# Kernel optimization log

Hardware: AMD Instinct MI355X
Metric: run time of the kernel (lower is better)

## Reference

```python
import jax, jax.numpy as jnp
import numpy as np

B, T, IN_DIM, OUT_DIM, H = 4096, 256, 64, 32, 128

def _linear_params(key, out_f, in_f):
    k1, k2 = jax.random.split(key)
    bound = 1.0 / np.sqrt(in_f)
    W = jax.random.uniform(k1, (out_f, in_f), jnp.float32, -bound, bound)
    b = jax.random.uniform(k2, (out_f,), jnp.float32, -bound, bound)
    return W, b

def _lstm_params(key, input_sz, hidden_sz):
    ks = jax.random.split(key, 4)
    bound = 1.0 / np.sqrt(hidden_sz)
    Wih = jax.random.uniform(ks[0], (4 * hidden_sz, input_sz), jnp.float32, -bound, bound)
    Whh = jax.random.uniform(ks[1], (4 * hidden_sz, hidden_sz), jnp.float32, -bound, bound)
    bih = jax.random.uniform(ks[2], (4 * hidden_sz,), jnp.float32, -bound, bound)
    bhh = jax.random.uniform(ks[3], (4 * hidden_sz,), jnp.float32, -bound, bound)
    return Wih, Whh, bih, bhh

def setup_inputs() -> dict:
    key = jax.random.key(0)
    ks = jax.random.split(key, 9)
    seq = jax.random.normal(ks[0], (B, T, IN_DIM), jnp.float32)
    h1 = jnp.zeros((B, H), jnp.float32); c1 = jnp.zeros((B, H), jnp.float32)
    h2 = jnp.zeros((B, H), jnp.float32); c2 = jnp.zeros((B, H), jnp.float32)
    W_in1, b_in1 = _linear_params(ks[1], 256, IN_DIM)
    W_in2, b_in2 = _linear_params(ks[2], 128, 256)
    W_in3, b_in3 = _linear_params(ks[3], 128, 128)
    Wih1, Whh1, bih1, bhh1 = _lstm_params(ks[4], 128, H)
    Wih2, Whh2, bih2, bhh2 = _lstm_params(ks[5], 128, H)
    W_out1, b_out1 = _linear_params(ks[6], 128, 128)
    W_out2, b_out2 = _linear_params(ks[7], 256, 128)
    W_out3, b_out3 = _linear_params(ks[8], OUT_DIM, 256)
    return dict(seq=seq, h1=h1, c1=c1, h2=h2, c2=c2,
                W_in1=W_in1, b_in1=b_in1, W_in2=W_in2, b_in2=b_in2, W_in3=W_in3, b_in3=b_in3,
                Wih1=Wih1, Whh1=Whh1, bih1=bih1, bhh1=bhh1,
                Wih2=Wih2, Whh2=Whh2, bih2=bih2, bhh2=bhh2,
                W_out1=W_out1, b_out1=b_out1, W_out2=W_out2, b_out2=b_out2, W_out3=W_out3, b_out3=b_out3)

def _lstm_cell(x, h, c, Wih, Whh, bih, bhh):
    # PyTorch LSTMCell: gates ordered i, f, g, o
    g = x @ Wih.T + bih + h @ Whh.T + bhh
    i, f, gg, o = jnp.split(g, 4, axis=-1)
    c_new = jax.nn.sigmoid(f) * c + jax.nn.sigmoid(i) * jnp.tanh(gg)
    h_new = jax.nn.sigmoid(o) * jnp.tanh(c_new)
    return h_new, c_new

def reference(seq, h1, c1, h2, c2,
              W_in1, b_in1, W_in2, b_in2, W_in3, b_in3,
              Wih1, Whh1, bih1, bhh1, Wih2, Whh2, bih2, bhh2,
              W_out1, b_out1, W_out2, b_out2, W_out3, b_out3):
    # fc_in applied to all timesteps at once (same math as per-step)
    x = jax.nn.relu(seq @ W_in1.T + b_in1)
    x = jax.nn.relu(x @ W_in2.T + b_in2)
    x = jax.nn.relu(x @ W_in3.T + b_in3)  # [B, T, 128]

    def step(carry, xt):
        h1, c1, h2, c2 = carry
        h1, c1 = _lstm_cell(xt, h1, c1, Wih1, Whh1, bih1, bhh1)
        h2, c2 = _lstm_cell(h1, h2, c2, Wih2, Whh2, bih2, bhh2)
        return (h1, c1, h2, c2), None

    (h1, c1, h2, c2), _ = jax.lax.scan(step, (h1, c1, h2, c2), jnp.swapaxes(x, 0, 1))

    y = jax.nn.relu(h2 @ W_out1.T + b_out1)
    y = jax.nn.relu(y @ W_out2.T + b_out2)
    return y @ W_out3.T + b_out3  # [B, out_dim]
```

## Files before the change

### kernel.cpp

```cpp
#include <hip/hip_runtime.h>


typedef unsigned short u16;
typedef short bf16x8 __attribute__((ext_vector_type(8)));
typedef float f32x4 __attribute__((ext_vector_type(4)));
typedef unsigned short u16x4 __attribute__((ext_vector_type(4)));

#define MFMA16(a, b, c) __builtin_amdgcn_mfma_f32_16x16x32_bf16((a), (b), (c), 0, 0, 0)

#define GLOAD_LDS(gp, lp) __builtin_amdgcn_global_load_lds( \
    (const __attribute__((address_space(1))) unsigned int*)(const void*)(gp), \
    (__attribute__((address_space(3))) unsigned int*)(void*)(lp), 16, 0, 0)

#define LGKM_BAR do { \
  asm volatile("s_waitcnt lgkmcnt(0)" ::: "memory"); \
  __builtin_amdgcn_sched_barrier(0); \
  __builtin_amdgcn_s_barrier(); \
  __builtin_amdgcn_sched_barrier(0); \
} while (0)

__device__ __forceinline__ u16 f2bf(float f) {
  union { float f; unsigned u; } v; v.f = f;
  return (u16)((v.u + 0x7FFFu + ((v.u >> 16) & 1u)) >> 16);
}
__device__ __forceinline__ float fsig(float x) { return 1.0f / (1.0f + __expf(-x)); }
__device__ __forceinline__ float ftanh(float x) { return 2.0f / (1.0f + __expf(-2.0f * x)) - 1.0f; }

#define WC1_U   0
#define WC2V_U  131072
#define WC2L_U  196608
#define W1_U    262144
#define W2_U    278528
#define W3_U    311296
#define WO1_U   327680
#define WO2_U   344064
#define WO3_U   376832
#define BS1_F   192512
#define BS2_F   193024
#define STH1_U  393216
#define STH2_U  917504
#define C1_F    720896
#define C2_F    1245184
#define XB_U    4194304
#define TC      32
#define NCH     8

__global__ void prep_kernel(const float* __restrict__ Wih1, const float* __restrict__ Whh1,
                            const float* __restrict__ bih1, const float* __restrict__ bhh1,
                            const float* __restrict__ Wih2, const float* __restrict__ Whh2,
                            const float* __restrict__ bih2, const float* __restrict__ bhh2,
                            const float* __restrict__ W_in1, const float* __restrict__ W_in2,
                            const float* __restrict__ W_in3,
                            const float* __restrict__ W_out1, const float* __restrict__ W_out2,
                            const float* __restrict__ W_out3,
                            const float* __restrict__ h1_in, const float* __restrict__ h2_in,
                            const float* __restrict__ c1_in, const float* __restrict__ c2_in,
                            u16* __restrict__ wsu) {
  float* wsf = (float*)wsu;
  const int N_total = 2490368;
  int stride = gridDim.x * blockDim.x;
  for (int idx = blockIdx.x * blockDim.x + threadIdx.x; idx < N_total; idx += stride) {
    if (idx < 385024) {
      int within = idx & 511;
      int frag = (idx >> 9);
      int lane = within >> 3, e = within & 7;
      int lr = lane & 15, lg = lane >> 4;
      int k8 = lg * 8 + e;
      float v;
      if (idx < 131072) {
        int kf = frag & 7, g = (frag >> 3) & 3, w = frag >> 5;
        int row = g * 128 + w * 16 + lr;
        int k = kf * 32 + k8;
        v = (k < 128) ? Wih1[row * 128 + k] : Whh1[row * 128 + (k - 128)];
      } else if (idx < 196608) {
        int f = frag - 256;
        int kf = f & 3, g = (f >> 2) & 3, w = f >> 4;
        v = Wih2[(g * 128 + w * 16 + lr) * 128 + kf * 32 + k8];
      } else if (idx < 262144) {
        int f = frag - 384;
        int kf = f & 3, g = (f >> 2) & 3, w = f >> 4;
        v = Whh2[(g * 128 + w * 16 + lr) * 128 + kf * 32 + k8];
      } else if (idx < 278528) {
        int f = frag - 512; int kf = f & 1, n = f >> 1;
        v = W_in1[(n * 16 + lr) * 64 + kf * 32 + k8];
      } else if (idx < 311296) {
        int f = frag - 544; int kf = f & 7, n = f >> 3;
        v = W_in2[(n * 16 + lr) * 256 + kf * 32 + k8];
      } else if (idx < 327680) {
        int f = frag - 608; int kf = f & 3, n = f >> 2;
        v = W_in3[(n * 16 + lr) * 128 + kf * 32 + k8];
      } else if (idx < 344064) {
        int f = frag - 640; int kf = f & 3, n = f >> 2;
        v = W_out1[(n * 16 + lr) * 128 + kf * 32 + k8];
      } else if (idx < 376832) {
        int f = frag - 672; int kf = f & 3, n = f >> 2;
        v = W_out2[(n * 16 + lr) * 128 + kf * 32 + k8];
      } else {
        int f = frag - 736; int kf = f & 7, n = f >> 3;
        v = W_out3[(n * 16 + lr) * 256 + kf * 32 + k8];
      }
      wsu[idx] = f2bf(v);
    } else if (idx < 385536) {
      int i = idx - 385024; wsf[BS1_F + i] = bih1[i] + bhh1[i];
    } else if (idx < 386048) {
      int i = idx - 385536; wsf[BS2_F + i] = bih2[i] + bhh2[i];
    } else if (idx < 393216) {
    } else if (idx < 917504) {
      int i = idx - 393216; wsu[STH1_U + i] = f2bf(h1_in[i]);
    } else if (idx < 1441792) {
      int i = idx - 917504; wsu[STH2_U + i] = f2bf(h2_in[i]);
    } else if (idx < 1966080) {
      int i = idx - 1441792; wsf[C1_F + i] = c1_in[i];
    } else {
      int i = idx - 1966080; wsf[C2_F + i] = c2_in[i];
    }
  }
}

__global__ __launch_bounds__(256, 2)
void fc_chunk(const float* __restrict__ seq,
              const float* __restrict__ b_in1, const float* __restrict__ b_in2,
              const float* __restrict__ b_in3,
              u16* __restrict__ wsu, int t0) {
  __shared__ u16 SEQs[4096];
  __shared__ u16 F1s[16384];
  __shared__ u16 F2s[8192];
  const int tid = threadIdx.x;
  const int wid = tid >> 6, lane = tid & 63;
  const int lr = lane & 15, lg = lane >> 4;
  const int bid = blockIdx.x;

#pragma unroll
  for (int i = 0; i < 4; ++i) {
    int f = i * 1024 + tid * 4;
    int rho = f >> 6, k = f & 63;
    int b = bid * 2 + (rho >> 5), tl = rho & 31;
    float4 v = *(const float4*)(seq + ((size_t)b * 256 + t0 + tl) * 64 + k);
    u16x4 o = { f2bf(v.x), f2bf(v.y), f2bf(v.z), f2bf(v.w) };
    *(u16x4*)&SEQs[(rho * 64 + k) ^ ((rho & 7) << 3)] = o;
  }
  __syncthreads();

  {
    f32x4 a1[4][4] = {};
#pragma unroll
    for (int kf = 0; kf < 2; ++kf) {
      bf16x8 A[4];
#pragma unroll
      for (int rt = 0; rt < 4; ++rt) {
        int r = 16 * rt + lr;
        A[rt] = *(const bf16x8*)&SEQs[(r * 64 + (kf * 4 + lg) * 8) ^ ((r & 7) << 3)];
      }
#pragma unroll
      for (int n = 0; n < 4; ++n) {
        bf16x8 B = *(const bf16x8*)(wsu + W1_U + (size_t)(((4 * wid + n) * 2 + kf) * 512) + lane * 8);
#pragma unroll
        for (int rt = 0; rt < 4; ++rt) a1[rt][n] = MFMA16(A[rt], B, a1[rt][n]);
      }
    }
#pragma unroll
    for (int n = 0; n < 4; ++n) {
      float bb = b_in1[(4 * wid + n) * 16 + lr];
#pragma unroll
      for (int rt = 0; rt < 4; ++rt)
#pragma unroll
        for (int j = 0; j < 4; ++j) {
          int r = 16 * rt + lg * 4 + j, c = (4 * wid + n) * 16 + lr;
          F1s[(r * 256 + c) ^ ((r & 7) << 3)] = f2bf(fmaxf(a1[rt][n][j] + bb, 0.f));
        }
    }
  }
  __syncthreads();

  {
    f32x4 a2[4][2] = {};
#pragma unroll
    for (int kf = 0; kf < 8; ++kf) {
      bf16x8 A[4];
#pragma unroll
      for (int rt = 0; rt < 4; ++rt) {
        int r = 16 * rt + lr;
        A[rt] = *(const bf16x8*)&F1s[(r * 256 + (kf * 4 + lg) * 8) ^ ((r & 7) << 3)];
      }
#pragma unroll
      for (int n = 0; n < 2; ++n) {
        bf16x8 B = *(const bf16x8*)(wsu + W2_U + (size_t)(((2 * wid + n) * 8 + kf) * 512) + lane * 8);
#pragma unroll
        for (int rt = 0; rt < 4; ++rt) a2[rt][n] = MFMA16(A[rt], B, a2[rt][n]);
      }
    }
#pragma unroll
    for (int n = 0; n < 2; ++n) {
      float bb = b_in2[(2 * wid + n) * 16 + lr];
#pragma unroll
      for (int rt = 0; rt < 4; ++rt)
#pragma unroll
        for (int j = 0; j < 4; ++j) {
          int r = 16 * rt + lg * 4 + j, c = (2 * wid + n) * 16 + lr;
          F2s[(r * 128 + c) ^ ((r & 7) << 3)] = f2bf(fmaxf(a2[rt][n][j] + bb, 0.f));
        }
    }
  }
  __syncthreads();

  {
    f32x4 a3[4][2] = {};
#pragma unroll
    for (int kf = 0; kf < 4; ++kf) {
      bf16x8 A[4];
#pragma unroll
      for (int rt = 0; rt < 4; ++rt) {
        int r = 16 * rt + lr;
        A[rt] = *(const bf16x8*)&F2s[(r * 128 + (kf * 4 + lg) * 8) ^ ((r & 7) << 3)];
      }
#pragma unroll
      for (int n = 0; n < 2; ++n) {
        bf16x8 B = *(const bf16x8*)(wsu + W3_U + (size_t)(((2 * wid + n) * 4 + kf) * 512) + lane * 8);
#pragma unroll
        for (int rt = 0; rt < 4; ++rt) a3[rt][n] = MFMA16(A[rt], B, a3[rt][n]);
      }
    }
#pragma unroll
    for (int n = 0; n < 2; ++n) {
      float bb = b_in3[(2 * wid + n) * 16 + lr];
#pragma unroll
      for (int rt = 0; rt < 4; ++rt)
#pragma unroll
        for (int j = 0; j < 4; ++j) {
          int rho = 16 * rt + lg * 4 + j;
          int b = bid * 2 + (rho >> 5), tl = rho & 31;
          int c = (2 * wid + n) * 16 + lr;
          wsu[XB_U + ((size_t)tl * 4096 + b) * 128 + c] = f2bf(fmaxf(a3[rt][n][j] + bb, 0.f));
        }
    }
  }
}

__global__ __launch_bounds__(512, 2)
void scan_chunk(u16* __restrict__ wsu, float* __restrict__ out,
                const float* __restrict__ b_out1, const float* __restrict__ b_out2,
                const float* __restrict__ b_out3, int last) {
  __shared__ u16 Wl[65536];
  __shared__ u16 XBs[2048];
  __shared__ u16 H1d[2][2048], H2d[2][2048];

  float* wsf = (float*)wsu;
  const int tid = threadIdx.x;
  const int wid = tid >> 6, lane = tid & 63;
  const int lr = lane & 15, lg = lane >> 4;
  const int b0 = blockIdx.x * 16;
  const int r5 = tid >> 5, c5 = (tid & 31) * 4;

  bf16x8 wgt1[4][8], wgt2v[4][4];
#pragma unroll
  for (int g = 0; g < 4; ++g) {
#pragma unroll
    for (int kf = 0; kf < 8; ++kf)
      wgt1[g][kf] = *(const bf16x8*)(wsu + WC1_U + (size_t)(((wid * 4 + g) * 8 + kf) * 512) + lane * 8);
#pragma unroll
    for (int kf = 0; kf < 4; ++kf)
      wgt2v[g][kf] = *(const bf16x8*)(wsu + WC2V_U + (size_t)(((wid * 4 + g) * 4 + kf) * 512) + lane * 8);
  }
#pragma unroll
  for (int g = 0; g < 4; ++g) {
#pragma unroll
    for (int kf = 0; kf < 8; ++kf) asm volatile("" : "+v"(wgt1[g][kf]));
#pragma unroll
    for (int kf = 0; kf < 4; ++kf) asm volatile("" : "+v"(wgt2v[g][kf]));
  }

#pragma unroll
  for (int i = 0; i < 16; ++i)
    GLOAD_LDS(wsu + WC2L_U + wid * 8192 + i * 512 + lane * 8, &Wl[wid * 8192 + i * 512]);

  u16x4 hh1 = *(const u16x4*)(wsu + STH1_U + (size_t)(b0 + r5) * 128 + c5);
  u16x4 hh2 = *(const u16x4*)(wsu + STH2_U + (size_t)(b0 + r5) * 128 + c5);
  u16x4 xq  = *(const u16x4*)(wsu + XB_U + ((size_t)0 * 4096 + b0 + r5) * 128 + c5);
  float cs1[4], cs2[4], bc1[4], bc2[4];
#pragma unroll
  for (int j = 0; j < 4; ++j) {
    cs1[j] = wsf[C1_F + (size_t)(b0 + lg * 4 + j) * 128 + 16 * wid + lr];
    cs2[j] = wsf[C2_F + (size_t)(b0 + lg * 4 + j) * 128 + 16 * wid + lr];
  }
#pragma unroll
  for (int g = 0; g < 4; ++g) {
    bc1[g] = wsf[BS1_F + g * 128 + 16 * wid + lr];
    bc2[g] = wsf[BS2_F + g * 128 + 16 * wid + lr];
  }
  {
    int sw = (r5 * 128 + c5) ^ ((r5 & 7) << 3);
    *(u16x4*)&H1d[0][sw] = hh1;
    *(u16x4*)&H2d[0][sw] = hh2;
    *(u16x4*)&XBs[sw] = xq;
  }
  __syncthreads();

#pragma unroll 2
  for (int tl = 0; tl < TC; ++tl) {
    const int p = tl & 1, q = p ^ 1;
    const bool ld = (tl < TC - 1);
    u16x4 xn;
    if (ld) xn = *(const u16x4*)(wsu + XB_U + ((size_t)(tl + 1) * 4096 + b0 + r5) * 128 + c5);

    f32x4 acc[4] = {};
#pragma unroll
    for (int kf = 0; kf < 8; ++kf) {
      const u16* ab = (kf < 4) ? XBs : H1d[p];
      int kg = (kf & 3) * 4 + lg;
      bf16x8 A = *(const bf16x8*)&ab[(lr * 128 + kg * 8) ^ ((lr & 7) << 3)];
#pragma unroll
      for (int g = 0; g < 4; ++g) acc[g] = MFMA16(A, wgt1[g][kf], acc[g]);
    }
    u16 hv[4];
#pragma unroll
    for (int j = 0; j < 4; ++j) {
      float gi = acc[0][j] + bc1[0];
      float gf = acc[1][j] + bc1[1];
      float gg = acc[2][j] + bc1[2];
      float go = acc[3][j] + bc1[3];
      float cn = fsig(gf) * cs1[j] + fsig(gi) * ftanh(gg);
      cs1[j] = cn;
      hv[j] = f2bf(fsig(go) * ftanh(cn));
    }
#pragma unroll
    for (int j = 0; j < 4; ++j) {
      int r = lg * 4 + j;
      H1d[q][(r * 128 + 16 * wid + lr) ^ ((r & 7) << 3)] = hv[j];
    }
    LGKM_BAR;

    f32x4 acd[4] = {};
#pragma unroll
    for (int kf = 0; kf < 4; ++kf) {
      int kg = kf * 4 + lg;
      bf16x8 A = *(const bf16x8*)&H1d[q][(lr * 128 + kg * 8) ^ ((lr & 7) << 3)];
#pragma unroll
      for (int g = 0; g < 4; ++g) acd[g] = MFMA16(A, wgt2v[g][kf], acd[g]);
    }
#pragma unroll
    for (int kf = 0; kf < 4; ++kf) {
      int kg = kf * 4 + lg;
      bf16x8 A = *(const bf16x8*)&H2d[p][(lr * 128 + kg * 8) ^ ((lr & 7) << 3)];
#pragma unroll
      for (int g = 0; g < 4; ++g) {
        bf16x8 B = *(const bf16x8*)&Wl[(size_t)(((wid * 4 + g) * 4 + kf) * 512) + lane * 8];
        acd[g] = MFMA16(A, B, acd[g]);
      }
    }
#pragma unroll
    for (int j = 0; j < 4; ++j) {
      float gi = acd[0][j] + bc2[0];
      float gf = acd[1][j] + bc2[1];
      float gg = acd[2][j] + bc2[2];
      float go = acd[3][j] + bc2[3];
      float cn = fsig(gf) * cs2[j] + fsig(gi) * ftanh(gg);
      cs2[j] = cn;
      hv[j] = f2bf(fsig(go) * ftanh(cn));
    }
#pragma unroll
    for (int j = 0; j < 4; ++j) {
      int r = lg * 4 + j;
      H2d[q][(r * 128 + 16 * wid + lr) ^ ((r & 7) << 3)] = hv[j];
    }
    if (ld) *(u16x4*)&XBs[(r5 * 128 + c5) ^ ((r5 & 7) << 3)] = xn;
    LGKM_BAR;
  }

  if (!last) {
    int sw = (r5 * 128 + c5) ^ ((r5 & 7) << 3);
    *(u16x4*)(wsu + STH1_U + (size_t)(b0 + r5) * 128 + c5) = *(const u16x4*)&H1d[0][sw];
    *(u16x4*)(wsu + STH2_U + (size_t)(b0 + r5) * 128 + c5) = *(const u16x4*)&H2d[0][sw];
#pragma unroll
    for (int j = 0; j < 4; ++j) {
      wsf[C1_F + (size_t)(b0 + lg * 4 + j) * 128 + 16 * wid + lr] = cs1[j];
      wsf[C2_F + (size_t)(b0 + lg * 4 + j) * 128 + 16 * wid + lr] = cs2[j];
    }
  } else {
    {
      f32x4 y1 = {};
#pragma unroll
      for (int kf = 0; kf < 4; ++kf) {
        int kg = kf * 4 + lg;
        bf16x8 A = *(const bf16x8*)&H2d[0][(lr * 128 + kg * 8) ^ ((lr & 7) << 3)];
        bf16x8 B = *(const bf16x8*)(wsu + WO1_U + (size_t)((wid * 4 + kf) * 512) + lane * 8);
        y1 = MFMA16(A, B, y1);
      }
      float bo1 = b_out1[wid * 16 + lr];
      LGKM_BAR;
#pragma unroll
      for (int j = 0; j < 4; ++j) {
        int r = lg * 4 + j;
        XBs[(r * 128 + 16 * wid + lr) ^ ((r & 7) << 3)] = f2bf(fmaxf(y1[j] + bo1, 0.f));
      }
      LGKM_BAR;
    }
    {
      f32x4 y2[2] = {};
#pragma unroll
      for (int kf = 0; kf < 4; ++kf) {
        int kg = kf * 4 + lg;
        bf16x8 A = *(const bf16x8*)&XBs[(lr * 128 + kg * 8) ^ ((lr & 7) << 3)];
#pragma unroll
        for (int n = 0; n < 2; ++n) {
          bf16x8 B = *(const bf16x8*)(wsu + WO2_U + (size_t)(((2 * wid + n) * 4 + kf) * 512) + lane * 8);
          y2[n] = MFMA16(A, B, y2[n]);
        }
      }
      LGKM_BAR;
#pragma unroll
      for (int n = 0; n < 2; ++n)
#pragma unroll
        for (int j = 0; j < 4; ++j) {
          int c = (2 * wid + n) * 16 + lr;
          float v = fmaxf(y2[n][j] + b_out2[c], 0.f);
          u16* buf = (c < 128) ? XBs : &H1d[0][0];
          int cc = c & 127, r = lg * 4 + j;
          buf[(r * 128 + cc) ^ ((r & 7) << 3)] = f2bf(v);
        }
      LGKM_BAR;
    }
    if (wid < 2) {
      f32x4 y3 = {};
#pragma unroll
      for (int kf = 0; kf < 8; ++kf) {
        const u16* ab = (kf < 4) ? XBs : &H1d[0][0];
        int kg = (kf & 3) * 4 + lg;
        bf16x8 A = *(const bf16x8*)&ab[(lr * 128 + kg * 8) ^ ((lr & 7) << 3)];
        bf16x8 B = *(const bf16x8*)(wsu + WO3_U + (size_t)((wid * 8 + kf) * 512) + lane * 8);
        y3 = MFMA16(A, B, y3);
      }
      float bo3 = b_out3[wid * 16 + lr];
#pragma unroll
      for (int j = 0; j < 4; ++j)
        out[(size_t)(b0 + lg * 4 + j) * 32 + wid * 16 + lr] = y3[j] + bo3;
    }
  }
}

extern "C" void kernel_launch(void* const* d_in, const int* in_sizes, int n_in,
                              void* d_out, int out_size, void* d_ws, size_t ws_size,
                              hipStream_t stream) {
  (void)in_sizes; (void)n_in; (void)out_size; (void)ws_size;
  const float* seq    = (const float*)d_in[0];
  const float* h1     = (const float*)d_in[1];
  const float* c1     = (const float*)d_in[2];
  const float* h2     = (const float*)d_in[3];
  const float* c2     = (const float*)d_in[4];
  const float* W_in1  = (const float*)d_in[5];
  const float* b_in1  = (const float*)d_in[6];
  const float* W_in2  = (const float*)d_in[7];
  const float* b_in2  = (const float*)d_in[8];
  const float* W_in3  = (const float*)d_in[9];
  const float* b_in3  = (const float*)d_in[10];
  const float* Wih1   = (const float*)d_in[11];
  const float* Whh1   = (const float*)d_in[12];
  const float* bih1   = (const float*)d_in[13];
  const float* bhh1   = (const float*)d_in[14];
  const float* Wih2   = (const float*)d_in[15];
  const float* Whh2   = (const float*)d_in[16];
  const float* bih2   = (const float*)d_in[17];
  const float* bhh2   = (const float*)d_in[18];
  const float* W_out1 = (const float*)d_in[19];
  const float* b_out1 = (const float*)d_in[20];
  const float* W_out2 = (const float*)d_in[21];
  const float* b_out2 = (const float*)d_in[22];
  const float* W_out3 = (const float*)d_in[23];
  const float* b_out3 = (const float*)d_in[24];
  u16* wsu = (u16*)d_ws;
  float* out = (float*)d_out;

  hipLaunchKernelGGL(prep_kernel, dim3(512), dim3(256), 0, stream,
                     Wih1, Whh1, bih1, bhh1, Wih2, Whh2, bih2, bhh2,
                     W_in1, W_in2, W_in3, W_out1, W_out2, W_out3,
                     h1, h2, c1, c2, wsu);
  for (int k = 0; k < NCH; ++k) {
    hipLaunchKernelGGL(fc_chunk, dim3(2048), dim3(256), 0, stream,
                       seq, b_in1, b_in2, b_in3, wsu, k * TC);
    hipLaunchKernelGGL(scan_chunk, dim3(256), dim3(512), 0, stream,
                       wsu, out, b_out1, b_out2, b_out3, (k == NCH - 1) ? 1 : 0);
  }
}
```

Before: 1.609 ms.

## Skew LSTM layers across timesteps to halve per-step barriers

Restructures the recurrent loop so layer 2 at step t and layer 1 at step t+1 run in the same iteration. Both read the same h1 fragments, so one barrier per timestep suffices instead of two, with a prologue and epilogue handling the first and last steps. X is double-buffered and prefetched two steps ahead, biases are folded into the accumulator initial values, and launch bounds drop to one block per CU, giving the compiler more registers. The risk is lower occupancy, added register pressure from holding h1 fragments across the skewed computation, and the complexity of the edge handling.

Result: slower. 2.096 ms (+30.3%).

```diff
diff --git a/kernel.cpp b/kernel.cpp
--- a/kernel.cpp
+++ b/kernel.cpp
@@ -236,13 +236,13 @@
   }
 }
 
-__global__ __launch_bounds__(512, 2)
+__global__ __launch_bounds__(512, 1)
 void scan_chunk(u16* __restrict__ wsu, float* __restrict__ out,
                 const float* __restrict__ b_out1, const float* __restrict__ b_out2,
                 const float* __restrict__ b_out3, int last) {
   __shared__ u16 Wl[65536];
-  __shared__ u16 XBs[2048];
-  __shared__ u16 H1d[2][2048], H2d[2][2048];
+  __shared__ u16 XB[2][2048];
+  __shared__ u16 H1b[2][2048], H2b[2][2048];
 
   float* wsf = (float*)wsu;
   const int tid = threadIdx.x;
@@ -250,6 +250,7 @@
   const int lr = lane & 15, lg = lane >> 4;
   const int b0 = blockIdx.x * 16;
   const int r5 = tid >> 5, c5 = (tid & 31) * 4;
+  const int swl = (r5 * 128 + c5) ^ ((r5 & 7) << 3);
 
   bf16x8 wgt1[4][8], wgt2v[4][4];
 #pragma unroll
@@ -273,9 +274,11 @@
   for (int i = 0; i < 16; ++i)
     GLOAD_LDS(wsu + WC2L_U + wid * 8192 + i * 512 + lane * 8, &Wl[wid * 8192 + i * 512]);
 
-  u16x4 hh1 = *(const u16x4*)(wsu + STH1_U + (size_t)(b0 + r5) * 128 + c5);
-  u16x4 hh2 = *(const u16x4*)(wsu + STH2_U + (size_t)(b0 + r5) * 128 + c5);
-  u16x4 xq  = *(const u16x4*)(wsu + XB_U + ((size_t)0 * 4096 + b0 + r5) * 128 + c5);
+  *(u16x4*)&H1b[0][swl] = *(const u16x4*)(wsu + STH1_U + (size_t)(b0 + r5) * 128 + c5);
+  *(u16x4*)&H2b[1][swl] = *(const u16x4*)(wsu + STH2_U + (size_t)(b0 + r5) * 128 + c5);
+  *(u16x4*)&XB[0][swl]  = *(const u16x4*)(wsu + XB_U + ((size_t)0 * 4096 + b0 + r5) * 128 + c5);
+  *(u16x4*)&XB[1][swl]  = *(const u16x4*)(wsu + XB_U + ((size_t)1 * 4096 + b0 + r5) * 128 + c5);
+
   float cs1[4], cs2[4], bc1[4], bc2[4];
 #pragma unroll
   for (int j = 0; j < 4; ++j) {
@@ -287,152 +290,191 @@
     bc1[g] = wsf[BS1_F + g * 128 + 16 * wid + lr];
     bc2[g] = wsf[BS2_F + g * 128 + 16 * wid + lr];
   }
-  {
-    int sw = (r5 * 128 + c5) ^ ((r5 & 7) << 3);
-    *(u16x4*)&H1d[0][sw] = hh1;
-    *(u16x4*)&H2d[0][sw] = hh2;
-    *(u16x4*)&XBs[sw] = xq;
-  }
   __syncthreads();
 
-#pragma unroll 2
-  for (int tl = 0; tl < TC; ++tl) {
-    const int p = tl & 1, q = p ^ 1;
-    const bool ld = (tl < TC - 1);
-    u16x4 xn;
-    if (ld) xn = *(const u16x4*)(wsu + XB_U + ((size_t)(tl + 1) * 4096 + b0 + r5) * 128 + c5);
-
-    f32x4 acc[4] = {};
-#pragma unroll
-    for (int kf = 0; kf < 8; ++kf) {
-      const u16* ab = (kf < 4) ? XBs : H1d[p];
-      int kg = (kf & 3) * 4 + lg;
-      bf16x8 A = *(const bf16x8*)&ab[(lr * 128 + kg * 8) ^ ((lr & 7) << 3)];
-#pragma unroll
-      for (int g = 0; g < 4; ++g) acc[g] = MFMA16(A, wgt1[g][kf], acc[g]);
-    }
-    u16 hv[4];
+  auto frag = [&](const u16* buf, int kg) -> bf16x8 {
+    return *(const bf16x8*)&buf[(lr * 128 + kg * 8) ^ ((lr & 7) << 3)];
+  };
+  auto ew = [&](f32x4 (&a)[4], float (&cs)[4], u16 (&hv)[4]) {
 #pragma unroll
     for (int j = 0; j < 4; ++j) {
-      float gi = acc[0][j] + bc1[0];
-      float gf = acc[1][j] + bc1[1];
-      float gg = acc[2][j] + bc1[2];
-      float go = acc[3][j] + bc1[3];
-      float cn = fsig(gf) * cs1[j] + fsig(gi) * ftanh(gg);
-      cs1[j] = cn;
-      hv[j] = f2bf(fsig(go) * ftanh(cn));
-    }
+      float cn = fsig(a[1][j]) * cs[j] + fsig(a[0][j]) * ftanh(a[2][j]);
+      cs[j] = cn;
+      hv[j] = f2bf(fsig(a[3][j]) * ftanh(cn));
+    }
+  };
+  auto hwrite = [&](u16* buf, const u16 (&hv)[4]) {
 #pragma unroll
     for (int j = 0; j < 4; ++j) {
       int r = lg * 4 + j;
-      H1d[q][(r * 128 + 16 * wid + lr) ^ ((r & 7) << 3)] = hv[j];
-    }
+      buf[(r * 128 + 16 * wid + lr) ^ ((r & 7) << 3)] = hv[j];
+    }
+  };
+
+  {
+    f32x4 a1[4];
+#pragma unroll
+    for (int g = 0; g < 4; ++g) a1[g] = (f32x4){bc1[g], bc1[g], bc1[g], bc1[g]};
+    bf16x8 h1f[4];
+#pragma unroll
+    for (int kf = 0; kf < 4; ++kf) h1f[kf] = frag(H1b[0], kf * 4 + lg);
+#pragma unroll
+    for (int kf = 0; kf < 4; ++kf) {
+      bf16x8 xf = frag(XB[0], kf * 4 + lg);
+#pragma unroll
+      for (int g = 0; g < 4; ++g) a1[g] = MFMA16(xf, wgt1[g][kf], a1[g]);
+    }
+#pragma unroll
+    for (int kf = 0; kf < 4; ++kf)
+#pragma unroll
+      for (int g = 0; g < 4; ++g) a1[g] = MFMA16(h1f[kf], wgt1[g][4 + kf], a1[g]);
+    u16 hv[4];
+    ew(a1, cs1, hv);
     LGKM_BAR;
-
-    f32x4 acd[4] = {};
+    hwrite(H1b[0], hv);
+    LGKM_BAR;
+  }
+
+#pragma unroll 2
+  for (int tl = 0; tl < TC - 1; ++tl) {
+    const int p = tl & 1, q = p ^ 1;
+    int tn = tl + 2; if (tn > TC - 1) tn = TC - 1;
+    u16x4 xn = *(const u16x4*)(wsu + XB_U + ((size_t)tn * 4096 + b0 + r5) * 128 + c5);
+
+    bf16x8 h1f[4];
+#pragma unroll
+    for (int kf = 0; kf < 4; ++kf) h1f[kf] = frag(H1b[p], kf * 4 + lg);
+
+    f32x4 a2[4];
+#pragma unroll
+    for (int g = 0; g < 4; ++g) a2[g] = (f32x4){bc2[g], bc2[g], bc2[g], bc2[g]};
+#pragma unroll
+    for (int kf = 0; kf < 4; ++kf)
+#pragma unroll
+      for (int g = 0; g < 4; ++g) a2[g] = MFMA16(h1f[kf], wgt2v[g][kf], a2[g]);
 #pragma unroll
     for (int kf = 0; kf < 4; ++kf) {
-      int kg = kf * 4 + lg;
-      bf16x8 A = *(const bf16x8*)&H1d[q][(lr * 128 + kg * 8) ^ ((lr & 7) << 3)];
-#pragma unroll
-      for (int g = 0; g < 4; ++g) acd[g] = MFMA16(A, wgt2v[g][kf], acd[g]);
-    }
+      bf16x8 h2f = frag(H2b[q], kf * 4 + lg);
+#pragma unroll
+      for (int g = 0; g < 4; ++g) {
+        bf16x8 B = *(const bf16x8*)&Wl[(((wid * 4 + g) * 4 + kf) * 512) + lane * 8];
+        a2[g] = MFMA16(h2f, B, a2[g]);
+      }
+    }
+    u16 hv[4];
+    ew(a2, cs2, hv);
+    hwrite(H2b[p], hv);
+
+    f32x4 a1[4];
+#pragma unroll
+    for (int g = 0; g < 4; ++g) a1[g] = (f32x4){bc1[g], bc1[g], bc1[g], bc1[g]};
 #pragma unroll
     for (int kf = 0; kf < 4; ++kf) {
-      int kg = kf * 4 + lg;
-      bf16x8 A = *(const bf16x8*)&H2d[p][(lr * 128 + kg * 8) ^ ((lr & 7) << 3)];
+      bf16x8 xf = frag(XB[q], kf * 4 + lg);
+#pragma unroll
+      for (int g = 0; g < 4; ++g) a1[g] = MFMA16(xf, wgt1[g][kf], a1[g]);
+    }
+#pragma unroll
+    for (int kf = 0; kf < 4; ++kf)
+#pragma unroll
+      for (int g = 0; g < 4; ++g) a1[g] = MFMA16(h1f[kf], wgt1[g][4 + kf], a1[g]);
+    ew(a1, cs1, hv);
+    hwrite(H1b[q], hv);
+    *(u16x4*)&XB[p][swl] = xn;
+    LGKM_BAR;
+  }
+
+  {
+    bf16x8 h1f[4];
+#pragma unroll
+    for (int kf = 0; kf < 4; ++kf) h1f[kf] = frag(H1b[1], kf * 4 + lg);
+    f32x4 a2[4];
+#pragma unroll
+    for (int g = 0; g < 4; ++g) a2[g] = (f32x4){bc2[g], bc2[g], bc2[g], bc2[g]};
+#pragma unroll
+    for (int kf = 0; kf < 4; ++kf)
+#pragma unroll
+      for (int g = 0; g < 4; ++g) a2[g] = MFMA16(h1f[kf], wgt2v[g][kf], a2[g]);
+#pragma unroll
+    for (int kf = 0; kf < 4; ++kf) {
+      bf16x8 h2f = frag(H2b[0], kf * 4 + lg);
 #pragma unroll
       for (int g = 0; g < 4; ++g) {
-        bf16x8 B = *(const bf16x8*)&Wl[(size_t)(((wid * 4 + g) * 4 + kf) * 512) + lane * 8];
-        acd[g] = MFMA16(A, B, acd[g]);
-      }
-    }
-#pragma unroll
-    for (int j = 0; j < 4; ++j) {
-      float gi = acd[0][j] + bc2[0];
-      float gf = acd[1][j] + bc2[1];
-      float gg = acd[2][j] + bc2[2];
-      float go = acd[3][j] + bc2[3];
-      float cn = fsig(gf) * cs2[j] + fsig(gi) * ftanh(gg);
-      cs2[j] = cn;
-      hv[j] = f2bf(fsig(go) * ftanh(cn));
-    }
-#pragma unroll
-    for (int j = 0; j < 4; ++j) {
-      int r = lg * 4 + j;
-      H2d[q][(r * 128 + 16 * wid + lr) ^ ((r & 7) << 3)] = hv[j];
-    }
-    if (ld) *(u16x4*)&XBs[(r5 * 128 + c5) ^ ((r5 & 7) << 3)] = xn;
-    LGKM_BAR;
-  }
-
-  if (!last) {
-    int sw = (r5 * 128 + c5) ^ ((r5 & 7) << 3);
-    *(u16x4*)(wsu + STH1_U + (size_t)(b0 + r5) * 128 + c5) = *(const u16x4*)&H1d[0][sw];
-    *(u16x4*)(wsu + STH2_U + (size_t)(b0 + r5) * 128 + c5) = *(const u16x4*)&H2d[0][sw];
-#pragma unroll
-    for (int j = 0; j < 4; ++j) {
-      wsf[C1_F + (size_t)(b0 + lg * 4 + j) * 128 + 16 * wid + lr] = cs1[j];
-      wsf[C2_F + (size_t)(b0 + lg * 4 + j) * 128 + 16 * wid + lr] = cs2[j];
-    }
-  } else {
-    {
-      f32x4 y1 = {};
-#pragma unroll
-      for (int kf = 0; kf < 4; ++kf) {
-        int kg = kf * 4 + lg;
-        bf16x8 A = *(const bf16x8*)&H2d[0][(lr * 128 + kg * 8) ^ ((lr & 7) << 3)];
-        bf16x8 B = *(const bf16x8*)(wsu + WO1_U + (size_t)((wid * 4 + kf) * 512) + lane * 8);
-        y1 = MFMA16(A, B, y1);
-      }
-      float bo1 = b_out1[wid * 16 + lr];
+        bf16x8 B = *(const bf16x8*)&Wl[(((wid * 4 + g) * 4 + kf) * 512) + lane * 8];
+        a2[g] = MFMA16(h2f, B, a2[g]);
+      }
+    }
+    u16 hv[4];
+    ew(a2, cs2, hv);
+
+    if (!last) {
+#pragma unroll
+      for (int j = 0; j < 4; ++j)
+        wsu[STH2_U + (size_t)(b0 + lg * 4 + j) * 128 + 16 * wid + lr] = hv[j];
+      *(u16x4*)(wsu + STH1_U + (size_t)(b0 + r5) * 128 + c5) = *(const u16x4*)&H1b[1][swl];
+#pragma unroll
+      for (int j = 0; j < 4; ++j) {
+        wsf[C1_F + (size_t)(b0 + lg * 4 + j) * 128 + 16 * wid + lr] = cs1[j];
+        wsf[C2_F + (size_t)(b0 + lg * 4 + j) * 128 + 16 * wid + lr] = cs2[j];
+      }
+    } else {
+      hwrite(H2b[1], hv);
       LGKM_BAR;
-#pragma unroll
-      for (int j = 0; j < 4; ++j) {
-        int r = lg * 4 + j;
-        XBs[(r * 128 + 16 * wid + lr) ^ ((r & 7) << 3)] = f2bf(fmaxf(y1[j] + bo1, 0.f));
-      }
-      LGKM_BAR;
-    }
-    {
-      f32x4 y2[2] = {};
-#pragma unroll
-      for (int kf = 0; kf < 4; ++kf) {
-        int kg = kf * 4 + lg;
-        bf16x8 A = *(const bf16x8*)&XBs[(lr * 128 + kg * 8) ^ ((lr & 7) << 3)];
-#pragma unroll
-        for (int n = 0; n < 2; ++n) {
-          bf16x8 B = *(const bf16x8*)(wsu + WO2_U + (size_t)(((2 * wid + n) * 4 + kf) * 512) + lane * 8);
-          y2[n] = MFMA16(A, B, y2[n]);
-        }
-      }
-      LGKM_BAR;
-#pragma unroll
-      for (int n = 0; n < 2; ++n)
+      {
+        f32x4 y1 = {};
+#pragma unroll
+        for (int kf = 0; kf < 4; ++kf) {
+          bf16x8 A = frag(H2b[1], kf * 4 + lg);
+          bf16x8 B = *(const bf16x8*)(wsu + WO1_U + (size_t)((wid * 4 + kf) * 512) + lane * 8);
+          y1 = MFMA16(A, B, y1);
+        }
+        float bo1 = b_out1[wid * 16 + lr];
+        LGKM_BAR;
 #pragma unroll
         for (int j = 0; j < 4; ++j) {
-          int c = (2 * wid + n) * 16 + lr;
-          float v = fmaxf(y2[n][j] + b_out2[c], 0.f);
-          u16* buf = (c < 128) ? XBs : &H1d[0][0];
-          int cc = c & 127, r = lg * 4 + j;
-          buf[(r * 128 + cc) ^ ((r & 7) << 3)] = f2bf(v);
-        }
-      LGKM_BAR;
-    }
-    if (wid < 2) {
-      f32x4 y3 = {};
-#pragma unroll
-      for (int kf = 0; kf < 8; ++kf) {
-        const u16* ab = (kf < 4) ? XBs : &H1d[0][0];
-        int kg = (kf & 3) * 4 + lg;
-        bf16x8 A = *(const bf16x8*)&ab[(lr * 128 + kg * 8) ^ ((lr & 7) << 3)];
-        bf16x8 B = *(const bf16x8*)(wsu + WO3_U + (size_t)((wid * 8 + kf) * 512) + lane * 8);
-        y3 = MFMA16(A, B, y3);
-      }
-      float bo3 = b_out3[wid * 16 + lr];
-#pragma unroll
-      for (int j = 0; j < 4; ++j)
-        out[(size_t)(b0 + lg * 4 + j) * 32 + wid * 16 + lr] = y3[j] + bo3;
+          int r = lg * 4 + j;
+          XB[0][(r * 128 + 16 * wid + lr) ^ ((r & 7) << 3)] = f2bf(fmaxf(y1[j] + bo1, 0.f));
+        }
+        LGKM_BAR;
+      }
+      {
+        f32x4 y2[2] = {};
+#pragma unroll
+        for (int kf = 0; kf < 4; ++kf) {
+          bf16x8 A = frag(XB[0], kf * 4 + lg);
+#pragma unroll
+          for (int n = 0; n < 2; ++n) {
+            bf16x8 B = *(const bf16x8*)(wsu + WO2_U + (size_t)(((2 * wid + n) * 4 + kf) * 512) + lane * 8);
+            y2[n] = MFMA16(A, B, y2[n]);
+          }
+        }
+        LGKM_BAR;
+#pragma unroll
+        for (int n = 0; n < 2; ++n)
+#pragma unroll
+          for (int j = 0; j < 4; ++j) {
+            int c = (2 * wid + n) * 16 + lr;
+            float v = fmaxf(y2[n][j] + b_out2[c], 0.f);
+            u16* buf = (c < 128) ? &XB[0][0] : &H1b[0][0];
+            int cc = c & 127, r = lg * 4 + j;
+            buf[(r * 128 + cc) ^ ((r & 7) << 3)] = f2bf(v);
+          }
+        LGKM_BAR;
+      }
+      if (wid < 2) {
+        f32x4 y3 = {};
+#pragma unroll
+        for (int kf = 0; kf < 8; ++kf) {
+          const u16* ab = (kf < 4) ? &XB[0][0] : &H1b[0][0];
+          bf16x8 A = frag(ab, (kf & 3) * 4 + lg);
+          bf16x8 B = *(const bf16x8*)(wsu + WO3_U + (size_t)((wid * 8 + kf) * 512) + lane * 8);
+          y3 = MFMA16(A, B, y3);
+        }
+        float bo3 = b_out3[wid * 16 + lr];
+#pragma unroll
+        for (int j = 0; j < 4; ++j)
+          out[(size_t)(b0 + lg * 4 + j) * 32 + wid * 16 + lr] = y3[j] + bo3;
+      }
     }
   }
 }
```

## Precompute layer-1 input gate projections in the FC kernel, shrink the scan loop

Applied to the files above, without the earlier changes.

The x·Wih1ᵀ+bias term of the first LSTM layer moves out of the sequential scan and into the parallel fc_chunk kernel. fc_chunk now writes bf16 pre-activation gates in a layout matched to each scan wave's fragment. The scan then only does the h1·Whh1 MFMAs for layer 1, keeps its register-resident weights in AGPRs, and drops one barrier per timestep. In exchange, the gate inputs are rounded to bf16 and the workspace traffic grows (4× wider per timestep than the old x buffer), and scan occupancy is lowered to one block per CU.

Result: slower. 1.924 ms (+19.6%).

```diff
diff --git a/kernel.cpp b/kernel.cpp
--- a/kernel.cpp
+++ b/kernel.cpp
@@ -23,12 +23,16 @@
   union { float f; unsigned u; } v; v.f = f;
   return (u16)((v.u + 0x7FFFu + ((v.u >> 16) & 1u)) >> 16);
 }
+__device__ __forceinline__ float b2f(u16 v) {
+  union { unsigned u; float f; } x; x.u = ((unsigned)v) << 16; return x.f;
+}
 __device__ __forceinline__ float fsig(float x) { return 1.0f / (1.0f + __expf(-x)); }
 __device__ __forceinline__ float ftanh(float x) { return 2.0f / (1.0f + __expf(-2.0f * x)) - 1.0f; }
 
-#define WC1_U   0
-#define WC2V_U  131072
-#define WC2L_U  196608
+#define WHH1_U  0
+#define WIH2_U  65536
+#define WHH2_U  131072
+#define WIH1_U  196608
 #define W1_U    262144
 #define W2_U    278528
 #define W3_U    311296
@@ -41,9 +45,10 @@
 #define STH2_U  917504
 #define C1_F    720896
 #define C2_F    1245184
-#define XB_U    4194304
+#define G1X_U   4194304
 #define TC      32
 #define NCH     8
+
 
 __global__ void prep_kernel(const float* __restrict__ Wih1, const float* __restrict__ Whh1,
                             const float* __restrict__ bih1, const float* __restrict__ bhh1,
@@ -62,41 +67,40 @@
   for (int idx = blockIdx.x * blockDim.x + threadIdx.x; idx < N_total; idx += stride) {
     if (idx < 385024) {
       int within = idx & 511;
-      int frag = (idx >> 9);
+      int f = idx >> 9;
       int lane = within >> 3, e = within & 7;
       int lr = lane & 15, lg = lane >> 4;
       int k8 = lg * 8 + e;
       float v;
-      if (idx < 131072) {
-        int kf = frag & 7, g = (frag >> 3) & 3, w = frag >> 5;
-        int row = g * 128 + w * 16 + lr;
-        int k = kf * 32 + k8;
-        v = (k < 128) ? Wih1[row * 128 + k] : Whh1[row * 128 + (k - 128)];
-      } else if (idx < 196608) {
-        int f = frag - 256;
+      if (f < 128) {
         int kf = f & 3, g = (f >> 2) & 3, w = f >> 4;
+        v = Whh1[(g * 128 + w * 16 + lr) * 128 + kf * 32 + k8];
+      } else if (f < 256) {
+        int ff = f - 128; int kf = ff & 3, g = (ff >> 2) & 3, w = ff >> 4;
         v = Wih2[(g * 128 + w * 16 + lr) * 128 + kf * 32 + k8];
-      } else if (idx < 262144) {
-        int f = frag - 384;
-        int kf = f & 3, g = (f >> 2) & 3, w = f >> 4;
+      } else if (f < 384) {
+        int ff = f - 256; int kf = ff & 3, g = (ff >> 2) & 3, w = ff >> 4;
         v = Whh2[(g * 128 + w * 16 + lr) * 128 + kf * 32 + k8];
-      } else if (idx < 278528) {
-        int f = frag - 512; int kf = f & 1, n = f >> 1;
+      } else if (f < 512) {
+        int ff = f - 384; int kf = ff & 3, n = ff >> 2;
+        v = Wih1[(n * 16 + lr) * 128 + kf * 32 + k8];
+      } else if (f < 544) {
+        int ff = f - 512; int kf = ff & 1, n = ff >> 1;
         v = W_in1[(n * 16 + lr) * 64 + kf * 32 + k8];
-      } else if (idx < 311296) {
-        int f = frag - 544; int kf = f & 7, n = f >> 3;
+      } else if (f < 608) {
+        int ff = f - 544; int kf = ff & 7, n = ff >> 3;
         v = W_in2[(n * 16 + lr) * 256 + kf * 32 + k8];
-      } else if (idx < 327680) {
-        int f = frag - 608; int kf = f & 3, n = f >> 2;
+      } else if (f < 640) {
+        int ff = f - 608; int kf = ff & 3, n = ff >> 2;
         v = W_in3[(n * 16 + lr) * 128 + kf * 32 + k8];
-      } else if (idx < 344064) {
-        int f = frag - 640; int kf = f & 3, n = f >> 2;
+      } else if (f < 672) {
+        int ff = f - 640; int kf = ff & 3, n = ff >> 2;
         v = W_out1[(n * 16 + lr) * 128 + kf * 32 + k8];
-      } else if (idx < 376832) {
-        int f = frag - 672; int kf = f & 3, n = f >> 2;
+      } else if (f < 736) {
+        int ff = f - 672; int kf = ff & 3, n = ff >> 2;
         v = W_out2[(n * 16 + lr) * 128 + kf * 32 + k8];
       } else {
-        int f = frag - 736; int kf = f & 7, n = f >> 3;
+        int ff = f - 736; int kf = ff & 7, n = ff >> 3;
         v = W_out3[(n * 16 + lr) * 256 + kf * 32 + k8];
       }
       wsu[idx] = f2bf(v);
@@ -125,17 +129,20 @@
   __shared__ u16 SEQs[4096];
   __shared__ u16 F1s[16384];
   __shared__ u16 F2s[8192];
+  __shared__ u16 XLs[8192];
   const int tid = threadIdx.x;
   const int wid = tid >> 6, lane = tid & 63;
   const int lr = lane & 15, lg = lane >> 4;
-  const int bid = blockIdx.x;
+  const int bid_t = blockIdx.x & 1, bid_b = blockIdx.x >> 1;
+  const int b0c = bid_b * 4, t0c = t0 + bid_t * 16;
+  const float* bs1f = (const float*)wsu + BS1_F;
 
 #pragma unroll
   for (int i = 0; i < 4; ++i) {
     int f = i * 1024 + tid * 4;
     int rho = f >> 6, k = f & 63;
-    int b = bid * 2 + (rho >> 5), tl = rho & 31;
-    float4 v = *(const float4*)(seq + ((size_t)b * 256 + t0 + tl) * 64 + k);
+    int b = b0c + (rho >> 4), tt = t0c + (rho & 15);
+    float4 v = *(const float4*)(seq + ((size_t)b * 256 + tt) * 64 + k);
     u16x4 o = { f2bf(v.x), f2bf(v.y), f2bf(v.z), f2bf(v.w) };
     *(u16x4*)&SEQs[(rho * 64 + k) ^ ((rho & 7) << 3)] = o;
   }
@@ -227,21 +234,52 @@
       for (int rt = 0; rt < 4; ++rt)
 #pragma unroll
         for (int j = 0; j < 4; ++j) {
-          int rho = 16 * rt + lg * 4 + j;
-          int b = bid * 2 + (rho >> 5), tl = rho & 31;
-          int c = (2 * wid + n) * 16 + lr;
-          wsu[XB_U + ((size_t)tl * 4096 + b) * 128 + c] = f2bf(fmaxf(a3[rt][n][j] + bb, 0.f));
+          int r = 16 * rt + lg * 4 + j, c = (2 * wid + n) * 16 + lr;
+          XLs[(r * 128 + c) ^ ((r & 7) << 3)] = f2bf(fmaxf(a3[rt][n][j] + bb, 0.f));
         }
     }
   }
+  __syncthreads();
+
+  {
+    f32x4 a4[4][8] = {};
+#pragma unroll
+    for (int kf = 0; kf < 4; ++kf) {
+      bf16x8 A[4];
+#pragma unroll
+      for (int rt = 0; rt < 4; ++rt) {
+        int r = 16 * rt + lr;
+        A[rt] = *(const bf16x8*)&XLs[(r * 128 + (kf * 4 + lg) * 8) ^ ((r & 7) << 3)];
+      }
+#pragma unroll
+      for (int n = 0; n < 8; ++n) {
+        bf16x8 B = *(const bf16x8*)(wsu + WIH1_U + (size_t)(((wid * 8 + n) * 4 + kf) * 512) + lane * 8);
+#pragma unroll
+        for (int rt = 0; rt < 4; ++rt) a4[rt][n] = MFMA16(A[rt], B, a4[rt][n]);
+      }
+    }
+    const int blk = bid_b >> 2, slg = bid_b & 3;
+#pragma unroll
+    for (int n = 0; n < 8; ++n) {
+      float bb = bs1f[(wid * 8 + n) * 16 + lr];
+#pragma unroll
+      for (int j = 0; j < 4; ++j) {
+        int tl = bid_t * 16 + lg * 4 + j;
+        u16x4 o = { f2bf(a4[0][n][j] + bb), f2bf(a4[1][n][j] + bb),
+                    f2bf(a4[2][n][j] + bb), f2bf(a4[3][n][j] + bb) };
+        size_t au = (size_t)G1X_U +
+            ((((((size_t)tl * 256 + blk) * 4 + slg) * 4 + wid) * 8 + n) * 16 + lr) * 4;
+        *(u16x4*)(wsu + au) = o;
+      }
+    }
+  }
 }
 
-__global__ __launch_bounds__(512, 2)
+__global__ __launch_bounds__(512, 1)
 void scan_chunk(u16* __restrict__ wsu, float* __restrict__ out,
                 const float* __restrict__ b_out1, const float* __restrict__ b_out2,
                 const float* __restrict__ b_out3, int last) {
   __shared__ u16 Wl[65536];
-  __shared__ u16 XBs[2048];
   __shared__ u16 H1d[2][2048], H2d[2][2048];
 
   float* wsf = (float*)wsu;
@@ -249,78 +287,80 @@
   const int wid = tid >> 6, lane = tid & 63;
   const int lr = lane & 15, lg = lane >> 4;
   const int b0 = blockIdx.x * 16;
+  const int blkid = blockIdx.x;
   const int r5 = tid >> 5, c5 = (tid & 31) * 4;
-
-  bf16x8 wgt1[4][8], wgt2v[4][4];
-#pragma unroll
-  for (int g = 0; g < 4; ++g) {
-#pragma unroll
-    for (int kf = 0; kf < 8; ++kf)
-      wgt1[g][kf] = *(const bf16x8*)(wsu + WC1_U + (size_t)(((wid * 4 + g) * 8 + kf) * 512) + lane * 8);
-#pragma unroll
-    for (int kf = 0; kf < 4; ++kf)
-      wgt2v[g][kf] = *(const bf16x8*)(wsu + WC2V_U + (size_t)(((wid * 4 + g) * 4 + kf) * 512) + lane * 8);
-  }
-#pragma unroll
-  for (int g = 0; g < 4; ++g) {
-#pragma unroll
-    for (int kf = 0; kf < 8; ++kf) asm volatile("" : "+v"(wgt1[g][kf]));
-#pragma unroll
-    for (int kf = 0; kf < 4; ++kf) asm volatile("" : "+v"(wgt2v[g][kf]));
-  }
+  const int swl = (r5 * 128 + c5) ^ ((r5 & 7) << 3);
+
+  bf16x8 wA[4][4], wB[4][4];
+#pragma unroll
+  for (int g = 0; g < 4; ++g)
+#pragma unroll
+    for (int kf = 0; kf < 4; ++kf) {
+      wA[g][kf] = *(const bf16x8*)(wsu + WHH1_U + (size_t)(((wid * 4 + g) * 4 + kf) * 512) + lane * 8);
+      wB[g][kf] = *(const bf16x8*)(wsu + WIH2_U + (size_t)(((wid * 4 + g) * 4 + kf) * 512) + lane * 8);
+    }
+#pragma unroll
+  for (int g = 0; g < 4; ++g)
+#pragma unroll
+    for (int kf = 0; kf < 4; ++kf) {
+      asm volatile("" : "+a"(wA[g][kf]));
+      asm volatile("" : "+a"(wB[g][kf]));
+    }
 
 #pragma unroll
   for (int i = 0; i < 16; ++i)
-    GLOAD_LDS(wsu + WC2L_U + wid * 8192 + i * 512 + lane * 8, &Wl[wid * 8192 + i * 512]);
-
-  u16x4 hh1 = *(const u16x4*)(wsu + STH1_U + (size_t)(b0 + r5) * 128 + c5);
-  u16x4 hh2 = *(const u16x4*)(wsu + STH2_U + (size_t)(b0 + r5) * 128 + c5);
-  u16x4 xq  = *(const u16x4*)(wsu + XB_U + ((size_t)0 * 4096 + b0 + r5) * 128 + c5);
-  float cs1[4], cs2[4], bc1[4], bc2[4];
+    GLOAD_LDS(wsu + WHH2_U + wid * 8192 + i * 512 + lane * 8, &Wl[wid * 8192 + i * 512]);
+
+  *(u16x4*)&H1d[0][swl] = *(const u16x4*)(wsu + STH1_U + (size_t)(b0 + r5) * 128 + c5);
+  *(u16x4*)&H2d[0][swl] = *(const u16x4*)(wsu + STH2_U + (size_t)(b0 + r5) * 128 + c5);
+  float cs1[4], cs2[4], bc2[4];
 #pragma unroll
   for (int j = 0; j < 4; ++j) {
     cs1[j] = wsf[C1_F + (size_t)(b0 + lg * 4 + j) * 128 + 16 * wid + lr];
     cs2[j] = wsf[C2_F + (size_t)(b0 + lg * 4 + j) * 128 + 16 * wid + lr];
   }
 #pragma unroll
-  for (int g = 0; g < 4; ++g) {
-    bc1[g] = wsf[BS1_F + g * 128 + 16 * wid + lr];
-    bc2[g] = wsf[BS2_F + g * 128 + 16 * wid + lr];
-  }
-  {
-    int sw = (r5 * 128 + c5) ^ ((r5 & 7) << 3);
-    *(u16x4*)&H1d[0][sw] = hh1;
-    *(u16x4*)&H2d[0][sw] = hh2;
-    *(u16x4*)&XBs[sw] = xq;
-  }
+  for (int g = 0; g < 4; ++g) bc2[g] = wsf[BS2_F + g * 128 + 16 * wid + lr];
+
+  u16x4 gx[4];
+#pragma unroll
+  for (int g = 0; g < 4; ++g)
+    gx[g] = *(const u16x4*)(wsu + G1X_U +
+        ((((((size_t)0 * 256 + blkid) * 4 + lg) * 4 + g) * 8 + wid) * 16 + lr) * 4);
+
   __syncthreads();
+
+  auto frag = [&](const u16* buf, int kg) -> bf16x8 {
+    return *(const bf16x8*)&buf[(lr * 128 + kg * 8) ^ ((lr & 7) << 3)];
+  };
 
 #pragma unroll 2
   for (int tl = 0; tl < TC; ++tl) {
     const int p = tl & 1, q = p ^ 1;
-    const bool ld = (tl < TC - 1);
-    u16x4 xn;
-    if (ld) xn = *(const u16x4*)(wsu + XB_U + ((size_t)(tl + 1) * 4096 + b0 + r5) * 128 + c5);
-
-    f32x4 acc[4] = {};
-#pragma unroll
-    for (int kf = 0; kf < 8; ++kf) {
-      const u16* ab = (kf < 4) ? XBs : H1d[p];
-      int kg = (kf & 3) * 4 + lg;
-      bf16x8 A = *(const bf16x8*)&ab[(lr * 128 + kg * 8) ^ ((lr & 7) << 3)];
-#pragma unroll
-      for (int g = 0; g < 4; ++g) acc[g] = MFMA16(A, wgt1[g][kf], acc[g]);
-    }
+
+    f32x4 acc[4];
+#pragma unroll
+    for (int g = 0; g < 4; ++g)
+      acc[g] = (f32x4){ b2f(gx[g][0]), b2f(gx[g][1]), b2f(gx[g][2]), b2f(gx[g][3]) };
+    if (tl < TC - 1) {
+#pragma unroll
+      for (int g = 0; g < 4; ++g)
+        gx[g] = *(const u16x4*)(wsu + G1X_U +
+            ((((((size_t)(tl + 1) * 256 + blkid) * 4 + lg) * 4 + g) * 8 + wid) * 16 + lr) * 4);
+    }
+    bf16x8 h1f[4];
+#pragma unroll
+    for (int kf = 0; kf < 4; ++kf) h1f[kf] = frag(H1d[p], kf * 4 + lg);
+#pragma unroll
+    for (int kf = 0; kf < 4; ++kf)
+#pragma unroll
+      for (int g = 0; g < 4; ++g) acc[g] = MFMA16(h1f[kf], wA[g][kf], acc[g]);
     u16 hv[4];
 #pragma unroll
     for (int j = 0; j < 4; ++j) {
-      float gi = acc[0][j] + bc1[0];
-      float gf = acc[1][j] + bc1[1];
-      float gg = acc[2][j] + bc1[2];
-      float go = acc[3][j] + bc1[3];
-      float cn = fsig(gf) * cs1[j] + fsig(gi) * ftanh(gg);
+      float cn = fsig(acc[1][j]) * cs1[j] + fsig(acc[0][j]) * ftanh(acc[2][j]);
       cs1[j] = cn;
-      hv[j] = f2bf(fsig(go) * ftanh(cn));
+      hv[j] = f2bf(fsig(acc[3][j]) * ftanh(cn));
     }
 #pragma unroll
     for (int j = 0; j < 4; ++j) {
@@ -329,47 +369,41 @@
     }
     LGKM_BAR;
 
-    f32x4 acd[4] = {};
+    f32x4 acd[4];
+#pragma unroll
+    for (int g = 0; g < 4; ++g) acd[g] = (f32x4){ bc2[g], bc2[g], bc2[g], bc2[g] };
 #pragma unroll
     for (int kf = 0; kf < 4; ++kf) {
-      int kg = kf * 4 + lg;
-      bf16x8 A = *(const bf16x8*)&H1d[q][(lr * 128 + kg * 8) ^ ((lr & 7) << 3)];
-#pragma unroll
-      for (int g = 0; g < 4; ++g) acd[g] = MFMA16(A, wgt2v[g][kf], acd[g]);
+      bf16x8 h1n = frag(H1d[q], kf * 4 + lg);
+#pragma unroll
+      for (int g = 0; g < 4; ++g) acd[g] = MFMA16(h1n, wB[g][kf], acd[g]);
     }
 #pragma unroll
     for (int kf = 0; kf < 4; ++kf) {
-      int kg = kf * 4 + lg;
-      bf16x8 A = *(const bf16x8*)&H2d[p][(lr * 128 + kg * 8) ^ ((lr & 7) << 3)];
+      bf16x8 h2f = frag(H2d[p], kf * 4 + lg);
 #pragma unroll
       for (int g = 0; g < 4; ++g) {
-        bf16x8 B = *(const bf16x8*)&Wl[(size_t)(((wid * 4 + g) * 4 + kf) * 512) + lane * 8];
-        acd[g] = MFMA16(A, B, acd[g]);
+        bf16x8 B = *(const bf16x8*)&Wl[((wid * 16 + g * 4 + kf) * 512) + lane * 8];
+        acd[g] = MFMA16(h2f, B, acd[g]);
       }
     }
 #pragma unroll
     for (int j = 0; j < 4; ++j) {
-      float gi = acd[0][j] + bc2[0];
-      float gf = acd[1][j] + bc2[1];
-      float gg = acd[2][j] + bc2[2];
-      float go = acd[3][j] + bc2[3];
-      float cn = fsig(gf) * cs2[j] + fsig(gi) * ftanh(gg);
+      float cn = fsig(acd[1][j]) * cs2[j] + fsig(acd[0][j]) * ftanh(acd[2][j]);
       cs2[j] = cn;
-      hv[j] = f2bf(fsig(go) * ftanh(cn));
+      hv[j] = f2bf(fsig(acd[3][j]) * ftanh(cn));
     }
 #pragma unroll
     for (int j = 0; j < 4; ++j) {
       int r = lg * 4 + j;
       H2d[q][(r * 128 + 16 * wid + lr) ^ ((r & 7) << 3)] = hv[j];
     }
-    if (ld) *(u16x4*)&XBs[(r5 * 128 + c5) ^ ((r5 & 7) << 3)] = xn;
-    LGKM_BAR;
-  }
+  }
+  LGKM_BAR;
 
   if (!last) {
-    int sw = (r5 * 128 + c5) ^ ((r5 & 7) << 3);
-    *(u16x4*)(wsu + STH1_U + (size_t)(b0 + r5) * 128 + c5) = *(const u16x4*)&H1d[0][sw];
-    *(u16x4*)(wsu + STH2_U + (size_t)(b0 + r5) * 128 + c5) = *(const u16x4*)&H2d[0][sw];
+    *(u16x4*)(wsu + STH1_U + (size_t)(b0 + r5) * 128 + c5) = *(const u16x4*)&H1d[0][swl];
+    *(u16x4*)(wsu + STH2_U + (size_t)(b0 + r5) * 128 + c5) = *(const u16x4*)&H2d[0][swl];
 #pragma unroll
     for (int j = 0; j < 4; ++j) {
       wsf[C1_F + (size_t)(b0 + lg * 4 + j) * 128 + 16 * wid + lr] = cs1[j];
@@ -380,8 +414,7 @@
       f32x4 y1 = {};
 #pragma unroll
       for (int kf = 0; kf < 4; ++kf) {
-        int kg = kf * 4 + lg;
-        bf16x8 A = *(const bf16x8*)&H2d[0][(lr * 128 + kg * 8) ^ ((lr & 7) << 3)];
+        bf16x8 A = frag(H2d[0], kf * 4 + lg);
         bf16x8 B = *(const bf16x8*)(wsu + WO1_U + (size_t)((wid * 4 + kf) * 512) + lane * 8);
         y1 = MFMA16(A, B, y1);
       }
@@ -390,7 +423,7 @@
 #pragma unroll
       for (int j = 0; j < 4; ++j) {
         int r = lg * 4 + j;
-        XBs[(r * 128 + 16 * wid + lr) ^ ((r & 7) << 3)] = f2bf(fmaxf(y1[j] + bo1, 0.f));
+        H1d[1][(r * 128 + 16 * wid + lr) ^ ((r & 7) << 3)] = f2bf(fmaxf(y1[j] + bo1, 0.f));
       }
       LGKM_BAR;
     }
@@ -398,8 +431,7 @@
       f32x4 y2[2] = {};
 #pragma unroll
       for (int kf = 0; kf < 4; ++kf) {
-        int kg = kf * 4 + lg;
-        bf16x8 A = *(const bf16x8*)&XBs[(lr * 128 + kg * 8) ^ ((lr & 7) << 3)];
+        bf16x8 A = frag(H1d[1], kf * 4 + lg);
 #pragma unroll
         for (int n = 0; n < 2; ++n) {
           bf16x8 B = *(const bf16x8*)(wsu + WO2_U + (size_t)(((2 * wid + n) * 4 + kf) * 512) + lane * 8);
@@ -413,7 +445,7 @@
         for (int j = 0; j < 4; ++j) {
           int c = (2 * wid + n) * 16 + lr;
           float v = fmaxf(y2[n][j] + b_out2[c], 0.f);
-          u16* buf = (c < 128) ? XBs : &H1d[0][0];
+          u16* buf = (c < 128) ? &H2d[1][0] : &H1d[0][0];
           int cc = c & 127, r = lg * 4 + j;
           buf[(r * 128 + cc) ^ ((r & 7) << 3)] = f2bf(v);
         }
@@ -423,9 +455,8 @@
       f32x4 y3 = {};
 #pragma unroll
       for (int kf = 0; kf < 8; ++kf) {
-        const u16* ab = (kf < 4) ? XBs : &H1d[0][0];
-        int kg = (kf & 3) * 4 + lg;
-        bf16x8 A = *(const bf16x8*)&ab[(lr * 128 + kg * 8) ^ ((lr & 7) << 3)];
+        const u16* ab = (kf < 4) ? &H2d[1][0] : &H1d[0][0];
+        bf16x8 A = frag(ab, (kf & 3) * 4 + lg);
         bf16x8 B = *(const bf16x8*)(wsu + WO3_U + (size_t)((wid * 8 + kf) * 512) + lane * 8);
         y3 = MFMA16(A, B, y3);
       }
```
